# Kernel tuning notes

Measured on AMD Instinct MI355X. Metric: run time of the kernel, lower is better.

## Reference

```python
import jax, jax.numpy as jnp
import numpy as np

B, S_NEW, DIM = 32, 1, 4096
H, KV, HD = 32, 8, 128          # query heads, kv heads, head_dim
PREV = 2048                      # tokens already in the KV cache


def setup_inputs() -> dict:
    key = jax.random.key(0)
    ks = jax.random.split(key, 8)
    return {
        "x": jax.random.normal(ks[0], (B, S_NEW, DIM), jnp.float32),
        "wq": jax.random.normal(ks[1], (DIM, H * HD), jnp.float32) * 0.02,
        "wk": jax.random.normal(ks[2], (DIM, KV * HD), jnp.float32) * 0.02,
        "wv": jax.random.normal(ks[3], (DIM, KV * HD), jnp.float32) * 0.02,
        "wo": jax.random.normal(ks[4], (H * HD, DIM), jnp.float32) * 0.02,
        "cache_k": jax.random.normal(ks[5], (B, PREV, KV, HD), jnp.float32),
        "cache_v": jax.random.normal(ks[6], (B, PREV, KV, HD), jnp.float32),
        "freqs": jax.random.normal(ks[7], (S_NEW, HD // 2), jnp.float32),  # rotary angles (angle of freqs_cis)
    }


def _apply_rope(t, cos, sin):
    # t: [b, s, h, hd]; interleaved pairs as in torch.view_as_complex
    a = t[..., 0::2]
    b = t[..., 1::2]
    c = cos[None, :, None, :]
    s = sin[None, :, None, :]
    ra = a * c - b * s
    rb = a * s + b * c
    return jnp.stack([ra, rb], axis=-1).reshape(t.shape)


def reference(x, wq, wk, wv, wo, cache_k, cache_v, freqs):
    b, s, _ = x.shape  # s == 1 (decode)
    xq = (x @ wq).reshape(b, s, H, HD)
    xk = (x @ wk).reshape(b, s, KV, HD)
    xv = (x @ wv).reshape(b, s, KV, HD)

    cos, sin = jnp.cos(freqs), jnp.sin(freqs)
    xq = _apply_rope(xq, cos, sin)
    xk = _apply_rope(xk, cos, sin)

    # KV-cache append (update_cache_decode)
    k_full = jnp.concatenate([cache_k, xk], axis=1)  # [b, PREV+1, KV, hd]
    v_full = jnp.concatenate([cache_v, xv], axis=1)

    # GQA attention without materializing the expanded cache
    g = H // KV
    q = xq.reshape(b, KV, g, HD)  # s == 1 folded away
    scale = 1.0 / jnp.sqrt(jnp.asarray(HD, x.dtype))
    scores = jnp.einsum("bkgd,bskd->bkgs", q, k_full) * scale  # [b, KV, g, PREV+1]
    attn = jax.nn.softmax(scores, axis=-1)
    out = jnp.einsum("bkgs,bskd->bkgd", attn, v_full)  # [b, KV, g, hd]
    out = out.reshape(b, s, H * HD)
    return out @ wo
```

## Files before the change

### kernel.cpp

```cpp
#include <hip/hip_runtime.h>


#define WS_P1   0
#define WS_QKV  6291456
#define WS_ATTN 6488064
#define WS_P2   6619136
#define WS_PA   10813440

__global__ __launch_bounds__(256) void gemm_skinny(
    const float* __restrict__ X,
    const float* __restrict__ W0, int e0, int ld0,
    const float* __restrict__ W1, int e1, int ld1,
    const float* __restrict__ W2, int ld2,
    float* __restrict__ P, int Ntot)
{
    __shared__ float x_t[128][36];
    __shared__ float2 red[128][33];

    const int nb = blockIdx.x * 256;
    const float* W; int ld, noff;
    if (nb < e0)      { W = W0; ld = ld0; noff = 0;  }
    else if (nb < e1) { W = W1; ld = ld1; noff = e0; }
    else              { W = W2; ld = ld2; noff = e1; }

    const int k0  = blockIdx.y * 128;
    const int tid = threadIdx.x;
    const int cp  = tid & 127;
    const int kg  = tid >> 7;
    const int nn  = nb - noff + cp * 2;

    #pragma unroll
    for (int i = 0; i < 16; ++i) {
        int idx = tid + i * 256;
        int bb = idx >> 7, kk = idx & 127;
        x_t[kk][bb] = X[(size_t)bb * 4096 + k0 + kk];
    }
    __syncthreads();

    float2 acc[32];
    #pragma unroll
    for (int b = 0; b < 32; ++b) { acc[b].x = 0.f; acc[b].y = 0.f; }

    const float* Wp = W + (size_t)k0 * ld + nn;
    for (int kk0 = kg * 64; kk0 < kg * 64 + 64; kk0 += 8) {
        float2 w[8];
        #pragma unroll
        for (int u = 0; u < 8; ++u)
            w[u] = *(const float2*)&Wp[(size_t)(kk0 + u) * ld];
        #pragma unroll
        for (int u = 0; u < 8; ++u) {
            const float* xr = x_t[kk0 + u];
            #pragma unroll
            for (int bq = 0; bq < 8; ++bq) {
                float4 xv = *(const float4*)&xr[bq * 4];
                acc[bq*4+0].x += xv.x * w[u].x; acc[bq*4+0].y += xv.x * w[u].y;
                acc[bq*4+1].x += xv.y * w[u].x; acc[bq*4+1].y += xv.y * w[u].y;
                acc[bq*4+2].x += xv.z * w[u].x; acc[bq*4+2].y += xv.z * w[u].y;
                acc[bq*4+3].x += xv.w * w[u].x; acc[bq*4+3].y += xv.w * w[u].y;
            }
        }
    }

    if (kg == 1) {
        #pragma unroll
        for (int b = 0; b < 32; ++b) red[cp][b] = acc[b];
    }
    __syncthreads();
    if (kg == 0) {
        const int ks = blockIdx.y;
        #pragma unroll
        for (int b = 0; b < 32; ++b) {
            float2 o = red[cp][b];
            float2 v; v.x = acc[b].x + o.x; v.y = acc[b].y + o.y;
            *(float2*)&P[((size_t)ks * 32 + b) * Ntot + nb + cp * 2] = v;
        }
    }
}

__global__ __launch_bounds__(256) void reduce_rope(
    const float* __restrict__ P, const float* __restrict__ freqs,
    float* __restrict__ qkv)
{
    int t = blockIdx.x * 256 + threadIdx.x;
    int b = t / 3072;
    int cp = t - b * 3072;
    int n = cp * 2;
    float sx = 0.f, sy = 0.f;
    #pragma unroll
    for (int ks = 0; ks < 32; ++ks) {
        float2 v = *(const float2*)&P[((size_t)ks * 32 + b) * 6144 + n];
        sx += v.x; sy += v.y;
    }
    if (n < 5120) {
        int d = n & 127;
        float fr = freqs[d >> 1];
        float c = cosf(fr), s = sinf(fr);
        float ra = sx * c - sy * s;
        float rb = sx * s + sy * c;
        if (n < 4096) {
            const float sc = 0.08838834764831845f;
            ra *= sc; rb *= sc;
        }
        sx = ra; sy = rb;
    }
    float2 o; o.x = sx; o.y = sy;
    *(float2*)&qkv[(size_t)b * 6144 + n] = o;
}

__global__ __launch_bounds__(256, 4) void attn_split(
    const float* __restrict__ qkv,
    const float* __restrict__ ck, const float* __restrict__ cv,
    float* __restrict__ pa)
{
    __shared__ float sbuf[4096];
    __shared__ float pm[4], pl[4];

    const int blk = blockIdx.x;
    const int c   = blk & 3;
    const int kv  = (blk >> 2) & 7;
    const int b   = blk >> 5;
    const int tid = threadIdx.x;
    const int wave = tid >> 6, lane = tid & 63;
    const int psub = (lane >> 4) & 3, dl = lane & 15;
    const int s0 = c * 512;

    float q[4][8];
    {
        const float* qb = qkv + (size_t)b * 6144 + kv * 512 + dl * 8;
        #pragma unroll
        for (int h = 0; h < 4; ++h) {
            float4 a = *(const float4*)&qb[h * 128];
            float4 e = *(const float4*)&qb[h * 128 + 4];
            q[h][0]=a.x; q[h][1]=a.y; q[h][2]=a.z; q[h][3]=a.w;
            q[h][4]=e.x; q[h][5]=e.y; q[h][6]=e.z; q[h][7]=e.w;
        }
    }

    if (c == 3 && tid < 16) {
        const float* kr = qkv + (size_t)b * 6144 + 4096 + kv * 128 + dl * 8;
        float4 k0 = *(const float4*)kr;
        float4 k1 = *(const float4*)(kr + 4);
        float p[4];
        #pragma unroll
        for (int h = 0; h < 4; ++h) {
            p[h] = q[h][0]*k0.x + q[h][1]*k0.y + q[h][2]*k0.z + q[h][3]*k0.w
                 + q[h][4]*k1.x + q[h][5]*k1.y + q[h][6]*k1.z + q[h][7]*k1.w;
        }
        #pragma unroll
        for (int off = 1; off < 16; off <<= 1) {
            #pragma unroll
            for (int h = 0; h < 4; ++h) p[h] += __shfl_xor(p[h], off);
        }
        if (dl == 0) {
            #pragma unroll
            for (int h = 0; h < 4; ++h) sbuf[h * 520 + 512] = p[h];
        }
    }

    const float* kbase = ck + ((size_t)b * 2048 * 8 + kv) * 128
                            + (size_t)s0 * 1024;
    const int srow = wave * 4 + psub;
    for (int it0 = 0; it0 < 32; it0 += 4) {
        float4 kA[4][2];
        #pragma unroll
        for (int u = 0; u < 4; ++u) {
            const float* kr = kbase + (size_t)((it0 + u) * 16 + srow) * 1024 + dl * 8;
            kA[u][0] = *(const float4*)kr;
            kA[u][1] = *(const float4*)(kr + 4);
        }
        #pragma unroll
        for (int u = 0; u < 4; ++u) {
            int s = (it0 + u) * 16 + srow;
            float p[4];
            #pragma unroll
            for (int h = 0; h < 4; ++h) {
                p[h] = q[h][0]*kA[u][0].x + q[h][1]*kA[u][0].y
                     + q[h][2]*kA[u][0].z + q[h][3]*kA[u][0].w
                     + q[h][4]*kA[u][1].x + q[h][5]*kA[u][1].y
                     + q[h][6]*kA[u][1].z + q[h][7]*kA[u][1].w;
            }
            #pragma unroll
            for (int off = 1; off < 16; off <<= 1) {
                #pragma unroll
                for (int h = 0; h < 4; ++h) p[h] += __shfl_xor(p[h], off);
            }
            if (dl == 0) {
                #pragma unroll
                for (int h = 0; h < 4; ++h) sbuf[h * 520 + s] = p[h];
            }
        }
    }
    __syncthreads();

    {
        const int h = wave;
        const int nrow = (c == 3) ? 513 : 512;
        float m = -1e30f;
        for (int s = lane; s < nrow; s += 64) m = fmaxf(m, sbuf[h * 520 + s]);
        #pragma unroll
        for (int off = 1; off < 64; off <<= 1) m = fmaxf(m, __shfl_xor(m, off));
        float sum = 0.f;
        for (int s = lane; s < nrow; s += 64) {
            float p = __expf(sbuf[h * 520 + s] - m);
            sbuf[h * 520 + s] = p;
            sum += p;
        }
        #pragma unroll
        for (int off = 1; off < 64; off <<= 1) sum += __shfl_xor(sum, off);
        if (lane == 0) { pm[h] = m; pl[h] = sum; }
    }
    __syncthreads();

    const int grp = tid >> 5, l32 = tid & 31, d4 = l32 * 4;
    float4 acc[4];
    #pragma unroll
    for (int hh = 0; hh < 4; ++hh) { acc[hh].x=0.f; acc[hh].y=0.f; acc[hh].z=0.f; acc[hh].w=0.f; }
    const float* vbase = cv + ((size_t)b * 2048 * 8 + kv) * 128
                            + (size_t)s0 * 1024;
    for (int it = 0; it < 16; ++it) {
        float4 vv[4];
        float pp[4][4];
        #pragma unroll
        for (int j = 0; j < 4; ++j) {
            int s = it * 32 + j * 8 + grp;
            vv[j] = *(const float4*)&vbase[(size_t)s * 1024 + d4];
        }
        #pragma unroll
        for (int j = 0; j < 4; ++j) {
            int s = it * 32 + j * 8 + grp;
            #pragma unroll
            for (int hh = 0; hh < 4; ++hh) pp[j][hh] = sbuf[hh * 520 + s];
        }
        #pragma unroll
        for (int j = 0; j < 4; ++j) {
            #pragma unroll
            for (int hh = 0; hh < 4; ++hh) {
                acc[hh].x += pp[j][hh] * vv[j].x;
                acc[hh].y += pp[j][hh] * vv[j].y;
                acc[hh].z += pp[j][hh] * vv[j].z;
                acc[hh].w += pp[j][hh] * vv[j].w;
            }
        }
    }
    if (c == 3 && grp == 0) {
        const float* vr = qkv + (size_t)b * 6144 + 5120 + kv * 128;
        float4 v = *(const float4*)&vr[d4];
        #pragma unroll
        for (int hh = 0; hh < 4; ++hh) {
            float p = sbuf[hh * 520 + 512];
            acc[hh].x += p * v.x; acc[hh].y += p * v.y;
            acc[hh].z += p * v.z; acc[hh].w += p * v.w;
        }
    }
    __syncthreads();

    #pragma unroll
    for (int hh = 0; hh < 4; ++hh)
        *(float4*)&sbuf[grp * 512 + hh * 128 + d4] = acc[hh];
    __syncthreads();

    float* rec = pa + (size_t)blk * 520;
    for (int t = tid; t < 512; t += 256) {
        int hh = t >> 7, d = t & 127;
        float v = 0.f;
        #pragma unroll
        for (int g = 0; g < 8; ++g) v += sbuf[g * 512 + hh * 128 + d];
        rec[8 + hh * 128 + d] = v;
    }
    if (tid < 4) { rec[tid] = pm[tid]; rec[4 + tid] = pl[tid]; }
}

__global__ __launch_bounds__(128) void attn_combine(
    const float* __restrict__ pa, float* __restrict__ ao)
{
    __shared__ float w_[4][4];
    const int g = blockIdx.x;
    const int d = threadIdx.x;
    const float* rec = pa + (size_t)g * 4 * 520;

    if (d < 4) {
        float m0 = rec[0*520 + d], m1 = rec[1*520 + d];
        float m2 = rec[2*520 + d], m3 = rec[3*520 + d];
        float M = fmaxf(fmaxf(m0, m1), fmaxf(m2, m3));
        float e0 = __expf(m0 - M), e1 = __expf(m1 - M);
        float e2 = __expf(m2 - M), e3 = __expf(m3 - M);
        float L = rec[0*520 + 4 + d] * e0 + rec[1*520 + 4 + d] * e1
                + rec[2*520 + 4 + d] * e2 + rec[3*520 + 4 + d] * e3;
        float inv = 1.0f / L;
        w_[0][d] = e0 * inv; w_[1][d] = e1 * inv;
        w_[2][d] = e2 * inv; w_[3][d] = e3 * inv;
    }
    __syncthreads();

    #pragma unroll
    for (int h = 0; h < 4; ++h) {
        float v = 0.f;
        #pragma unroll
        for (int c = 0; c < 4; ++c)
            v += rec[c*520 + 8 + h*128 + d] * w_[c][h];
        ao[(size_t)g * 512 + h * 128 + d] = v;
    }
}

__global__ __launch_bounds__(256) void reduce_out(
    const float* __restrict__ P, float* __restrict__ out)
{
    int t = blockIdx.x * 256 + threadIdx.x;
    int b = t >> 11;
    int cp = t & 2047;
    int n = cp * 2;
    float sx = 0.f, sy = 0.f;
    #pragma unroll
    for (int ks = 0; ks < 32; ++ks) {
        float2 v = *(const float2*)&P[((size_t)ks * 32 + b) * 4096 + n];
        sx += v.x; sy += v.y;
    }
    float2 o; o.x = sx; o.y = sy;
    *(float2*)&out[(size_t)b * 4096 + n] = o;
}

extern "C" void kernel_launch(void* const* d_in, const int* in_sizes, int n_in,
                              void* d_out, int out_size, void* d_ws, size_t ws_size,
                              hipStream_t stream) {
    const float* x  = (const float*)d_in[0];
    const float* wq = (const float*)d_in[1];
    const float* wk = (const float*)d_in[2];
    const float* wv = (const float*)d_in[3];
    const float* wo = (const float*)d_in[4];
    const float* ck = (const float*)d_in[5];
    const float* cv = (const float*)d_in[6];
    const float* fr = (const float*)d_in[7];
    float* out = (float*)d_out;
    float* ws  = (float*)d_ws;

    float* P1   = ws + WS_P1;
    float* qkv  = ws + WS_QKV;
    float* attn = ws + WS_ATTN;
    float* P2   = ws + WS_P2;
    float* PA   = ws + WS_PA;

    dim3 g1(24, 32);
    gemm_skinny<<<g1, 256, 0, stream>>>(x, wq, 4096, 4096, wk, 5120, 1024,
                                        wv, 1024, P1, 6144);
    reduce_rope<<<384, 256, 0, stream>>>(P1, fr, qkv);
    attn_split<<<1024, 256, 0, stream>>>(qkv, ck, cv, PA);
    attn_combine<<<256, 128, 0, stream>>>(PA, attn);
    dim3 g4(16, 32);
    gemm_skinny<<<g4, 256, 0, stream>>>(attn, wo, 4096, 4096, wo, 4096, 4096,
                                        wo, 4096, P2, 4096);
    reduce_out<<<256, 256, 0, stream>>>(P2, out);
}
```

Measured before the change: 183.8 us.

## Restructure decode attention to split sequence per batch covering all KV heads

The attention kernel now gives each block a 128-token chunk of one batch across all 8 KV heads, so each cache row is read as one contiguous 4 KB line instead of a 512 B strided slice. Shuffle reductions shrink to 8 lanes, and a cross-wave reduction through shared memory replaces the per-group reduction. The combine step now merges 16 chunks instead of 4, and the partial buffer reuses the P1 workspace. The reduce kernels also move to 128-thread blocks. The cost is more registers and shared memory per block, fewer blocks (512), and a larger partial buffer to combine.

Result: slower. 190.5 us (+3.7%).

```diff
diff --git a/kernel.cpp b/kernel.cpp
--- a/kernel.cpp
+++ b/kernel.cpp
@@ -2,10 +2,10 @@
 
 
 #define WS_P1   0
+#define WS_PA   0
 #define WS_QKV  6291456
 #define WS_ATTN 6488064
 #define WS_P2   6619136
-#define WS_PA   10813440
 
 __global__ __launch_bounds__(256) void gemm_skinny(
     const float* __restrict__ X,
@@ -77,11 +77,11 @@
     }
 }
 
-__global__ __launch_bounds__(256) void reduce_rope(
+__global__ __launch_bounds__(128) void reduce_rope(
     const float* __restrict__ P, const float* __restrict__ freqs,
     float* __restrict__ qkv)
 {
-    int t = blockIdx.x * 256 + threadIdx.x;
+    int t = blockIdx.x * 128 + threadIdx.x;
     int b = t / 3072;
     int cp = t - b * 3072;
     int n = cp * 2;
@@ -107,188 +107,231 @@
     *(float2*)&qkv[(size_t)b * 6144 + n] = o;
 }
 
-__global__ __launch_bounds__(256, 4) void attn_split(
+__global__ __launch_bounds__(256, 2) void attn_seq(
     const float* __restrict__ qkv,
     const float* __restrict__ ck, const float* __restrict__ cv,
     float* __restrict__ pa)
 {
-    __shared__ float sbuf[4096];
-    __shared__ float pm[4], pl[4];
+    __shared__ float sc[32 * 133 + 3];
+    __shared__ float scratch[3 * 4160];
+    __shared__ float pm[32], pl[32];
 
     const int blk = blockIdx.x;
-    const int c   = blk & 3;
-    const int kv  = (blk >> 2) & 7;
-    const int b   = blk >> 5;
+    const int cnk = blk & 15;
+    const int b   = blk >> 4;
     const int tid = threadIdx.x;
-    const int wave = tid >> 6, lane = tid & 63;
-    const int psub = (lane >> 4) & 3, dl = lane & 15;
-    const int s0 = c * 512;
-
-    float q[4][8];
+    const int w   = tid >> 6, l = tid & 63;
+    const int kv  = l >> 3, jj = l & 7;
+    const bool tok = (cnk == 15) && (w == 3);
+
     {
-        const float* qb = qkv + (size_t)b * 6144 + kv * 512 + dl * 8;
-        #pragma unroll
-        for (int h = 0; h < 4; ++h) {
-            float4 a = *(const float4*)&qb[h * 128];
-            float4 e = *(const float4*)&qb[h * 128 + 4];
-            q[h][0]=a.x; q[h][1]=a.y; q[h][2]=a.z; q[h][3]=a.w;
-            q[h][4]=e.x; q[h][5]=e.y; q[h][6]=e.z; q[h][7]=e.w;
-        }
-    }
-
-    if (c == 3 && tid < 16) {
-        const float* kr = qkv + (size_t)b * 6144 + 4096 + kv * 128 + dl * 8;
-        float4 k0 = *(const float4*)kr;
-        float4 k1 = *(const float4*)(kr + 4);
-        float p[4];
-        #pragma unroll
-        for (int h = 0; h < 4; ++h) {
-            p[h] = q[h][0]*k0.x + q[h][1]*k0.y + q[h][2]*k0.z + q[h][3]*k0.w
-                 + q[h][4]*k1.x + q[h][5]*k1.y + q[h][6]*k1.z + q[h][7]*k1.w;
-        }
-        #pragma unroll
-        for (int off = 1; off < 16; off <<= 1) {
-            #pragma unroll
-            for (int h = 0; h < 4; ++h) p[h] += __shfl_xor(p[h], off);
-        }
-        if (dl == 0) {
-            #pragma unroll
-            for (int h = 0; h < 4; ++h) sbuf[h * 520 + 512] = p[h];
-        }
-    }
-
-    const float* kbase = ck + ((size_t)b * 2048 * 8 + kv) * 128
-                            + (size_t)s0 * 1024;
-    const int srow = wave * 4 + psub;
-    for (int it0 = 0; it0 < 32; it0 += 4) {
-        float4 kA[4][2];
-        #pragma unroll
-        for (int u = 0; u < 4; ++u) {
-            const float* kr = kbase + (size_t)((it0 + u) * 16 + srow) * 1024 + dl * 8;
-            kA[u][0] = *(const float4*)kr;
-            kA[u][1] = *(const float4*)(kr + 4);
-        }
-        #pragma unroll
-        for (int u = 0; u < 4; ++u) {
-            int s = (it0 + u) * 16 + srow;
+        const float* qb = qkv + (size_t)b * 6144 + tid * 16;
+        float4 t0 = *(const float4*)(qb);
+        float4 t1 = *(const float4*)(qb + 4);
+        float4 t2 = *(const float4*)(qb + 8);
+        float4 t3 = *(const float4*)(qb + 12);
+        *(float4*)&scratch[tid * 16]      = t0;
+        *(float4*)&scratch[tid * 16 + 4]  = t1;
+        *(float4*)&scratch[tid * 16 + 8]  = t2;
+        *(float4*)&scratch[tid * 16 + 12] = t3;
+    }
+    __syncthreads();
+    float4 q4[4][4];
+    #pragma unroll
+    for (int h = 0; h < 4; ++h) {
+        #pragma unroll
+        for (int u = 0; u < 4; ++u)
+            q4[h][u] = *(const float4*)&scratch[(kv * 4 + h) * 128 + jj * 16 + u * 4];
+    }
+
+    const float* kb_ = ck + ((size_t)b * 2048 + cnk * 128 + w * 32) * 1024 + l * 16;
+    for (int t = 0; t < 32; t += 2) {
+        float4 ka[2][4];
+        #pragma unroll
+        for (int r = 0; r < 2; ++r) {
+            #pragma unroll
+            for (int u = 0; u < 4; ++u)
+                ka[r][u] = *(const float4*)(kb_ + (size_t)(t + r) * 1024 + u * 4);
+        }
+        #pragma unroll
+        for (int r = 0; r < 2; ++r) {
             float p[4];
             #pragma unroll
             for (int h = 0; h < 4; ++h) {
-                p[h] = q[h][0]*kA[u][0].x + q[h][1]*kA[u][0].y
-                     + q[h][2]*kA[u][0].z + q[h][3]*kA[u][0].w
-                     + q[h][4]*kA[u][1].x + q[h][5]*kA[u][1].y
-                     + q[h][6]*kA[u][1].z + q[h][7]*kA[u][1].w;
-            }
-            #pragma unroll
-            for (int off = 1; off < 16; off <<= 1) {
+                p[h] = q4[h][0].x*ka[r][0].x + q4[h][0].y*ka[r][0].y
+                     + q4[h][0].z*ka[r][0].z + q4[h][0].w*ka[r][0].w
+                     + q4[h][1].x*ka[r][1].x + q4[h][1].y*ka[r][1].y
+                     + q4[h][1].z*ka[r][1].z + q4[h][1].w*ka[r][1].w
+                     + q4[h][2].x*ka[r][2].x + q4[h][2].y*ka[r][2].y
+                     + q4[h][2].z*ka[r][2].z + q4[h][2].w*ka[r][2].w
+                     + q4[h][3].x*ka[r][3].x + q4[h][3].y*ka[r][3].y
+                     + q4[h][3].z*ka[r][3].z + q4[h][3].w*ka[r][3].w;
+            }
+            #pragma unroll
+            for (int off = 1; off < 8; off <<= 1) {
                 #pragma unroll
                 for (int h = 0; h < 4; ++h) p[h] += __shfl_xor(p[h], off);
             }
-            if (dl == 0) {
+            if (jj == 0) {
                 #pragma unroll
-                for (int h = 0; h < 4; ++h) sbuf[h * 520 + s] = p[h];
-            }
+                for (int h = 0; h < 4; ++h)
+                    sc[(kv * 4 + h) * 133 + w * 32 + t + r] = p[h];
+            }
+        }
+    }
+    if (tok) {
+        const float* kr = qkv + (size_t)b * 6144 + 4096 + l * 16;
+        float4 ka[4];
+        #pragma unroll
+        for (int u = 0; u < 4; ++u) ka[u] = *(const float4*)(kr + u * 4);
+        float p[4];
+        #pragma unroll
+        for (int h = 0; h < 4; ++h) {
+            p[h] = q4[h][0].x*ka[0].x + q4[h][0].y*ka[0].y + q4[h][0].z*ka[0].z + q4[h][0].w*ka[0].w
+                 + q4[h][1].x*ka[1].x + q4[h][1].y*ka[1].y + q4[h][1].z*ka[1].z + q4[h][1].w*ka[1].w
+                 + q4[h][2].x*ka[2].x + q4[h][2].y*ka[2].y + q4[h][2].z*ka[2].z + q4[h][2].w*ka[2].w
+                 + q4[h][3].x*ka[3].x + q4[h][3].y*ka[3].y + q4[h][3].z*ka[3].z + q4[h][3].w*ka[3].w;
+        }
+        #pragma unroll
+        for (int off = 1; off < 8; off <<= 1) {
+            #pragma unroll
+            for (int h = 0; h < 4; ++h) p[h] += __shfl_xor(p[h], off);
+        }
+        if (jj == 0) {
+            #pragma unroll
+            for (int h = 0; h < 4; ++h) sc[(kv * 4 + h) * 133 + 128] = p[h];
         }
     }
     __syncthreads();
 
     {
-        const int h = wave;
-        const int nrow = (c == 3) ? 513 : 512;
+        const int kvh = w * 8 + (l >> 3);
+        const int j = l & 7;
+        const int nrow = (cnk == 15) ? 129 : 128;
         float m = -1e30f;
-        for (int s = lane; s < nrow; s += 64) m = fmaxf(m, sbuf[h * 520 + s]);
-        #pragma unroll
-        for (int off = 1; off < 64; off <<= 1) m = fmaxf(m, __shfl_xor(m, off));
+        for (int s = j; s < nrow; s += 8) m = fmaxf(m, sc[kvh * 133 + s]);
+        #pragma unroll
+        for (int off = 1; off < 8; off <<= 1) m = fmaxf(m, __shfl_xor(m, off));
         float sum = 0.f;
-        for (int s = lane; s < nrow; s += 64) {
-            float p = __expf(sbuf[h * 520 + s] - m);
-            sbuf[h * 520 + s] = p;
+        for (int s = j; s < nrow; s += 8) {
+            float p = __expf(sc[kvh * 133 + s] - m);
+            sc[kvh * 133 + s] = p;
             sum += p;
         }
         #pragma unroll
-        for (int off = 1; off < 64; off <<= 1) sum += __shfl_xor(sum, off);
-        if (lane == 0) { pm[h] = m; pl[h] = sum; }
-    }
-    __syncthreads();
-
-    const int grp = tid >> 5, l32 = tid & 31, d4 = l32 * 4;
-    float4 acc[4];
-    #pragma unroll
-    for (int hh = 0; hh < 4; ++hh) { acc[hh].x=0.f; acc[hh].y=0.f; acc[hh].z=0.f; acc[hh].w=0.f; }
-    const float* vbase = cv + ((size_t)b * 2048 * 8 + kv) * 128
-                            + (size_t)s0 * 1024;
-    for (int it = 0; it < 16; ++it) {
-        float4 vv[4];
-        float pp[4][4];
-        #pragma unroll
-        for (int j = 0; j < 4; ++j) {
-            int s = it * 32 + j * 8 + grp;
-            vv[j] = *(const float4*)&vbase[(size_t)s * 1024 + d4];
-        }
-        #pragma unroll
-        for (int j = 0; j < 4; ++j) {
-            int s = it * 32 + j * 8 + grp;
-            #pragma unroll
-            for (int hh = 0; hh < 4; ++hh) pp[j][hh] = sbuf[hh * 520 + s];
-        }
-        #pragma unroll
-        for (int j = 0; j < 4; ++j) {
-            #pragma unroll
-            for (int hh = 0; hh < 4; ++hh) {
-                acc[hh].x += pp[j][hh] * vv[j].x;
-                acc[hh].y += pp[j][hh] * vv[j].y;
-                acc[hh].z += pp[j][hh] * vv[j].z;
-                acc[hh].w += pp[j][hh] * vv[j].w;
-            }
-        }
-    }
-    if (c == 3 && grp == 0) {
-        const float* vr = qkv + (size_t)b * 6144 + 5120 + kv * 128;
-        float4 v = *(const float4*)&vr[d4];
-        #pragma unroll
-        for (int hh = 0; hh < 4; ++hh) {
-            float p = sbuf[hh * 520 + 512];
-            acc[hh].x += p * v.x; acc[hh].y += p * v.y;
-            acc[hh].z += p * v.z; acc[hh].w += p * v.w;
-        }
-    }
-    __syncthreads();
-
-    #pragma unroll
-    for (int hh = 0; hh < 4; ++hh)
-        *(float4*)&sbuf[grp * 512 + hh * 128 + d4] = acc[hh];
-    __syncthreads();
-
-    float* rec = pa + (size_t)blk * 520;
-    for (int t = tid; t < 512; t += 256) {
-        int hh = t >> 7, d = t & 127;
-        float v = 0.f;
-        #pragma unroll
-        for (int g = 0; g < 8; ++g) v += sbuf[g * 512 + hh * 128 + d];
-        rec[8 + hh * 128 + d] = v;
-    }
-    if (tid < 4) { rec[tid] = pm[tid]; rec[4 + tid] = pl[tid]; }
+        for (int off = 1; off < 8; off <<= 1) sum += __shfl_xor(sum, off);
+        if (j == 0) { pm[kvh] = m; pl[kvh] = sum; }
+    }
+    __syncthreads();
+
+    float4 a4[4][4];
+    #pragma unroll
+    for (int h = 0; h < 4; ++h) {
+        #pragma unroll
+        for (int u = 0; u < 4; ++u) { a4[h][u].x=0.f; a4[h][u].y=0.f; a4[h][u].z=0.f; a4[h][u].w=0.f; }
+    }
+    const float* vb_ = cv + ((size_t)b * 2048 + cnk * 128 + w * 32) * 1024 + l * 16;
+    for (int t = 0; t < 32; t += 2) {
+        float4 va[2][4];
+        #pragma unroll
+        for (int r = 0; r < 2; ++r) {
+            #pragma unroll
+            for (int u = 0; u < 4; ++u)
+                va[r][u] = *(const float4*)(vb_ + (size_t)(t + r) * 1024 + u * 4);
+        }
+        #pragma unroll
+        for (int r = 0; r < 2; ++r) {
+            const int row = w * 32 + t + r;
+            float p[4];
+            #pragma unroll
+            for (int h = 0; h < 4; ++h) p[h] = sc[(kv * 4 + h) * 133 + row];
+            #pragma unroll
+            for (int h = 0; h < 4; ++h) {
+                #pragma unroll
+                for (int u = 0; u < 4; ++u) {
+                    a4[h][u].x += p[h] * va[r][u].x;
+                    a4[h][u].y += p[h] * va[r][u].y;
+                    a4[h][u].z += p[h] * va[r][u].z;
+                    a4[h][u].w += p[h] * va[r][u].w;
+                }
+            }
+        }
+    }
+    if (tok) {
+        const float* vr = qkv + (size_t)b * 6144 + 5120 + l * 16;
+        float4 va[4];
+        #pragma unroll
+        for (int u = 0; u < 4; ++u) va[u] = *(const float4*)(vr + u * 4);
+        float p[4];
+        #pragma unroll
+        for (int h = 0; h < 4; ++h) p[h] = sc[(kv * 4 + h) * 133 + 128];
+        #pragma unroll
+        for (int h = 0; h < 4; ++h) {
+            #pragma unroll
+            for (int u = 0; u < 4; ++u) {
+                a4[h][u].x += p[h] * va[u].x;
+                a4[h][u].y += p[h] * va[u].y;
+                a4[h][u].z += p[h] * va[u].z;
+                a4[h][u].w += p[h] * va[u].w;
+            }
+        }
+    }
+    __syncthreads();
+
+    if (w > 0) {
+        float* dst = scratch + (w - 1) * 4160;
+        #pragma unroll
+        for (int h = 0; h < 4; ++h) {
+            #pragma unroll
+            for (int u = 0; u < 4; ++u)
+                *(float4*)&dst[(kv * 4 + h) * 128 + jj * 16 + u * 4] = a4[h][u];
+        }
+    }
+    __syncthreads();
+    float* rec = pa + (size_t)blk * 4160;
+    if (w == 0) {
+        #pragma unroll
+        for (int h = 0; h < 4; ++h) {
+            #pragma unroll
+            for (int u = 0; u < 4; ++u) {
+                float4 v = a4[h][u];
+                #pragma unroll
+                for (int ww = 0; ww < 3; ++ww) {
+                    float4 o = *(const float4*)&scratch[ww * 4160 + (kv * 4 + h) * 128 + jj * 16 + u * 4];
+                    v.x += o.x; v.y += o.y; v.z += o.z; v.w += o.w;
+                }
+                *(float4*)&rec[64 + (kv * 4 + h) * 128 + jj * 16 + u * 4] = v;
+            }
+        }
+    }
+    if (tid < 32) { rec[tid] = pm[tid]; rec[32 + tid] = pl[tid]; }
 }
 
 __global__ __launch_bounds__(128) void attn_combine(
     const float* __restrict__ pa, float* __restrict__ ao)
 {
-    __shared__ float w_[4][4];
+    __shared__ float wgt[16][4];
     const int g = blockIdx.x;
+    const int b = g >> 3, kv = g & 7;
     const int d = threadIdx.x;
-    const float* rec = pa + (size_t)g * 4 * 520;
+    const float* base = pa + (size_t)b * 16 * 4160;
 
     if (d < 4) {
-        float m0 = rec[0*520 + d], m1 = rec[1*520 + d];
-        float m2 = rec[2*520 + d], m3 = rec[3*520 + d];
-        float M = fmaxf(fmaxf(m0, m1), fmaxf(m2, m3));
-        float e0 = __expf(m0 - M), e1 = __expf(m1 - M);
-        float e2 = __expf(m2 - M), e3 = __expf(m3 - M);
-        float L = rec[0*520 + 4 + d] * e0 + rec[1*520 + 4 + d] * e1
-                + rec[2*520 + 4 + d] * e2 + rec[3*520 + 4 + d] * e3;
+        const int kvh = kv * 4 + d;
+        float M = -1e30f;
+        #pragma unroll
+        for (int c = 0; c < 16; ++c)
+            M = fmaxf(M, base[(size_t)c * 4160 + kvh]);
+        float L = 0.f;
+        float e[16];
+        #pragma unroll
+        for (int c = 0; c < 16; ++c) {
+            e[c] = __expf(base[(size_t)c * 4160 + kvh] - M);
+            L += base[(size_t)c * 4160 + 32 + kvh] * e[c];
+        }
         float inv = 1.0f / L;
-        w_[0][d] = e0 * inv; w_[1][d] = e1 * inv;
-        w_[2][d] = e2 * inv; w_[3][d] = e3 * inv;
+        #pragma unroll
+        for (int c = 0; c < 16; ++c) wgt[c][d] = e[c] * inv;
     }
     __syncthreads();
 
@@ -296,16 +339,16 @@
     for (int h = 0; h < 4; ++h) {
         float v = 0.f;
         #pragma unroll
-        for (int c = 0; c < 4; ++c)
-            v += rec[c*520 + 8 + h*128 + d] * w_[c][h];
-        ao[(size_t)g * 512 + h * 128 + d] = v;
-    }
-}
-
-__global__ __launch_bounds__(256) void reduce_out(
+        for (int c = 0; c < 16; ++c)
+            v += base[(size_t)c * 4160 + 64 + (kv * 4 + h) * 128 + d] * wgt[c][h];
+        ao[(size_t)b * 4096 + kv * 512 + h * 128 + d] = v;
+    }
+}
+
+__global__ __launch_bounds__(128) void reduce_out(
     const float* __restrict__ P, float* __restrict__ out)
 {
-    int t = blockIdx.x * 256 + threadIdx.x;
+    int t = blockIdx.x * 128 + threadIdx.x;
     int b = t >> 11;
     int cp = t & 2047;
     int n = cp * 2;
@@ -334,19 +377,19 @@
     float* ws  = (float*)d_ws;
 
     float* P1   = ws + WS_P1;
+    float* PA   = ws + WS_PA;
     float* qkv  = ws + WS_QKV;
     float* attn = ws + WS_ATTN;
     float* P2   = ws + WS_P2;
-    float* PA   = ws + WS_PA;
 
     dim3 g1(24, 32);
     gemm_skinny<<<g1, 256, 0, stream>>>(x, wq, 4096, 4096, wk, 5120, 1024,
                                         wv, 1024, P1, 6144);
-    reduce_rope<<<384, 256, 0, stream>>>(P1, fr, qkv);
-    attn_split<<<1024, 256, 0, stream>>>(qkv, ck, cv, PA);
+    reduce_rope<<<768, 128, 0, stream>>>(P1, fr, qkv);
+    attn_seq<<<512, 256, 0, stream>>>(qkv, ck, cv, PA);
     attn_combine<<<256, 128, 0, stream>>>(PA, attn);
     dim3 g4(16, 32);
     gemm_skinny<<<g4, 256, 0, stream>>>(attn, wo, 4096, 4096, wo, 4096, 4096,
                                         wo, 4096, P2, 4096);
-    reduce_out<<<256, 256, 0, stream>>>(P2, out);
-}
+    reduce_out<<<512, 128, 0, stream>>>(P2, out);
+}
```

## Restructure attention QK mapping so each thread handles one head-half per key row

Applied to the files above, without the earlier changes.

Remaps the QK score phase of the split attention kernel so that each group of 8 threads covers one key row: 4 heads by 2 halves, each thread holding 64 q values in registers. This replaces the 16-lane shuffle reduction across 4 heads with a single xor-4 shuffle, at the cost of higher register pressure and narrower per-thread K reads. It also reuses P1 workspace for the partial-attention buffer to shrink the workspace footprint, and halves the block size of the two reduction kernels while doubling their grid.

After: 234.2 us. +27.4%, slower.

```diff
diff --git a/kernel.cpp b/kernel.cpp
--- a/kernel.cpp
+++ b/kernel.cpp
@@ -2,10 +2,10 @@
 
 
 #define WS_P1   0
+#define WS_PA   0
 #define WS_QKV  6291456
 #define WS_ATTN 6488064
 #define WS_P2   6619136
-#define WS_PA   10813440
 
 __global__ __launch_bounds__(256) void gemm_skinny(
     const float* __restrict__ X,
@@ -77,11 +77,11 @@
     }
 }
 
-__global__ __launch_bounds__(256) void reduce_rope(
+__global__ __launch_bounds__(128) void reduce_rope(
     const float* __restrict__ P, const float* __restrict__ freqs,
     float* __restrict__ qkv)
 {
-    int t = blockIdx.x * 256 + threadIdx.x;
+    int t = blockIdx.x * 128 + threadIdx.x;
     int b = t / 3072;
     int cp = t - b * 3072;
     int n = cp * 2;
@@ -121,74 +121,50 @@
     const int b   = blk >> 5;
     const int tid = threadIdx.x;
     const int wave = tid >> 6, lane = tid & 63;
-    const int psub = (lane >> 4) & 3, dl = lane & 15;
     const int s0 = c * 512;
 
-    float q[4][8];
+    const int hh4  = tid & 3;
+    const int half = (tid >> 2) & 1;
+    const int rowg = tid >> 3;
+
+    float4 qreg[16];
     {
-        const float* qb = qkv + (size_t)b * 6144 + kv * 512 + dl * 8;
-        #pragma unroll
-        for (int h = 0; h < 4; ++h) {
-            float4 a = *(const float4*)&qb[h * 128];
-            float4 e = *(const float4*)&qb[h * 128 + 4];
-            q[h][0]=a.x; q[h][1]=a.y; q[h][2]=a.z; q[h][3]=a.w;
-            q[h][4]=e.x; q[h][5]=e.y; q[h][6]=e.z; q[h][7]=e.w;
-        }
-    }
-
-    if (c == 3 && tid < 16) {
-        const float* kr = qkv + (size_t)b * 6144 + 4096 + kv * 128 + dl * 8;
-        float4 k0 = *(const float4*)kr;
-        float4 k1 = *(const float4*)(kr + 4);
-        float p[4];
-        #pragma unroll
-        for (int h = 0; h < 4; ++h) {
-            p[h] = q[h][0]*k0.x + q[h][1]*k0.y + q[h][2]*k0.z + q[h][3]*k0.w
-                 + q[h][4]*k1.x + q[h][5]*k1.y + q[h][6]*k1.z + q[h][7]*k1.w;
-        }
-        #pragma unroll
-        for (int off = 1; off < 16; off <<= 1) {
-            #pragma unroll
-            for (int h = 0; h < 4; ++h) p[h] += __shfl_xor(p[h], off);
-        }
-        if (dl == 0) {
-            #pragma unroll
-            for (int h = 0; h < 4; ++h) sbuf[h * 520 + 512] = p[h];
-        }
-    }
-
-    const float* kbase = ck + ((size_t)b * 2048 * 8 + kv) * 128
-                            + (size_t)s0 * 1024;
-    const int srow = wave * 4 + psub;
-    for (int it0 = 0; it0 < 32; it0 += 4) {
-        float4 kA[4][2];
-        #pragma unroll
-        for (int u = 0; u < 4; ++u) {
-            const float* kr = kbase + (size_t)((it0 + u) * 16 + srow) * 1024 + dl * 8;
-            kA[u][0] = *(const float4*)kr;
-            kA[u][1] = *(const float4*)(kr + 4);
-        }
-        #pragma unroll
-        for (int u = 0; u < 4; ++u) {
-            int s = (it0 + u) * 16 + srow;
-            float p[4];
-            #pragma unroll
-            for (int h = 0; h < 4; ++h) {
-                p[h] = q[h][0]*kA[u][0].x + q[h][1]*kA[u][0].y
-                     + q[h][2]*kA[u][0].z + q[h][3]*kA[u][0].w
-                     + q[h][4]*kA[u][1].x + q[h][5]*kA[u][1].y
-                     + q[h][6]*kA[u][1].z + q[h][7]*kA[u][1].w;
+        const float* qb = qkv + (size_t)b * 6144 + kv * 512 + hh4 * 128 + half * 64;
+        #pragma unroll
+        for (int u = 0; u < 16; ++u) qreg[u] = *(const float4*)&qb[u * 4];
+    }
+
+    if (c == 3 && tid < 8) {
+        const float* kr = qkv + (size_t)b * 6144 + 4096 + kv * 128 + half * 64;
+        float p = 0.f;
+        #pragma unroll
+        for (int u = 0; u < 16; ++u) {
+            float4 ka = *(const float4*)&kr[u * 4];
+            p += qreg[u].x*ka.x + qreg[u].y*ka.y + qreg[u].z*ka.z + qreg[u].w*ka.w;
+        }
+        p += __shfl_xor(p, 4);
+        if (half == 0) sbuf[hh4 * 520 + 512] = p;
+    }
+
+    const float* kbase = ck + (((size_t)b * 2048 + s0) * 8 + kv) * 128 + half * 64;
+    for (int pass = 0; pass < 16; ++pass) {
+        const int s = pass * 32 + rowg;
+        const float* kr = kbase + (size_t)s * 1024;
+        float p = 0.f;
+        #pragma unroll
+        for (int g2 = 0; g2 < 2; ++g2) {
+            float4 ka[8];
+            #pragma unroll
+            for (int u = 0; u < 8; ++u)
+                ka[u] = *(const float4*)&kr[g2 * 32 + u * 4];
+            #pragma unroll
+            for (int u = 0; u < 8; ++u) {
+                float4 qv = qreg[g2 * 8 + u];
+                p += qv.x*ka[u].x + qv.y*ka[u].y + qv.z*ka[u].z + qv.w*ka[u].w;
             }
-            #pragma unroll
-            for (int off = 1; off < 16; off <<= 1) {
-                #pragma unroll
-                for (int h = 0; h < 4; ++h) p[h] += __shfl_xor(p[h], off);
-            }
-            if (dl == 0) {
-                #pragma unroll
-                for (int h = 0; h < 4; ++h) sbuf[h * 520 + s] = p[h];
-            }
-        }
+        }
+        p += __shfl_xor(p, 4);
+        if (half == 0) sbuf[hh4 * 520 + s] = p;
     }
     __syncthreads();
 
@@ -215,8 +191,7 @@
     float4 acc[4];
     #pragma unroll
     for (int hh = 0; hh < 4; ++hh) { acc[hh].x=0.f; acc[hh].y=0.f; acc[hh].z=0.f; acc[hh].w=0.f; }
-    const float* vbase = cv + ((size_t)b * 2048 * 8 + kv) * 128
-                            + (size_t)s0 * 1024;
+    const float* vbase = cv + (((size_t)b * 2048 + s0) * 8 + kv) * 128;
     for (int it = 0; it < 16; ++it) {
         float4 vv[4];
         float pp[4][4];
@@ -302,10 +277,10 @@
     }
 }
 
-__global__ __launch_bounds__(256) void reduce_out(
+__global__ __launch_bounds__(128) void reduce_out(
     const float* __restrict__ P, float* __restrict__ out)
 {
-    int t = blockIdx.x * 256 + threadIdx.x;
+    int t = blockIdx.x * 128 + threadIdx.x;
     int b = t >> 11;
     int cp = t & 2047;
     int n = cp * 2;
@@ -334,19 +309,19 @@
     float* ws  = (float*)d_ws;
 
     float* P1   = ws + WS_P1;
+    float* PA   = ws + WS_PA;
     float* qkv  = ws + WS_QKV;
     float* attn = ws + WS_ATTN;
     float* P2   = ws + WS_P2;
-    float* PA   = ws + WS_PA;
 
     dim3 g1(24, 32);
     gemm_skinny<<<g1, 256, 0, stream>>>(x, wq, 4096, 4096, wk, 5120, 1024,
                                         wv, 1024, P1, 6144);
-    reduce_rope<<<384, 256, 0, stream>>>(P1, fr, qkv);
+    reduce_rope<<<768, 128, 0, stream>>>(P1, fr, qkv);
     attn_split<<<1024, 256, 0, stream>>>(qkv, ck, cv, PA);
     attn_combine<<<256, 128, 0, stream>>>(PA, attn);
     dim3 g4(16, 32);
     gemm_skinny<<<g4, 256, 0, stream>>>(attn, wo, 4096, 4096, wo, 4096, 4096,
                                         wo, 4096, P2, 4096);
-    reduce_out<<<256, 256, 0, stream>>>(P2, out);
-}
+    reduce_out<<<512, 128, 0, stream>>>(P2, out);
+}
```
